# Optimization experiments

Hardware: AMD Instinct MI355X
Metric: run time of the kernel (lower is better)

## Reference

```python
import jax, jax.numpy as jnp
import numpy as np

COMMITMENT = 0.25  # beta


def setup_inputs() -> dict:
    key = jax.random.key(0)
    k1, k2 = jax.random.split(key)
    B, M, D, K = 16, 4096, 64, 1024
    z_e = jax.random.normal(k1, (B, M, D), dtype=jnp.float32)
    embed = jax.random.normal(k2, (K, D), dtype=jnp.float32)  # codebook C in R^{KxD}
    return {"z_e": z_e, "embed": embed}


def reference(z_e, embed):
    """Eval-mode VQ forward: nearest-code lookup + VQ loss + straight-through.

    z_e:   (B, M, D) encoder outputs
    embed: (K, D) codebook
    Returns (z_q_st, indices, vq_loss).
    """
    B, M, D = z_e.shape
    flat = z_e.reshape(-1, D)  # (N, D)
    dist = (
        jnp.sum(flat * flat, axis=1, keepdims=True)
        - 2.0 * (flat @ embed.T)
        + jnp.sum(embed * embed, axis=1)[None, :]
    )
    indices = jnp.argmin(dist, axis=1)  # (N,)
    z_q = embed[indices].reshape(B, M, D)  # gather

    sg = jax.lax.stop_gradient
    codebook_loss = jnp.mean((z_q - sg(z_e)) ** 2)
    commitment_loss = jnp.mean((z_e - sg(z_q)) ** 2)
    vq_loss = codebook_loss + COMMITMENT * commitment_loss

    z_q_st = z_e + sg(z_q - z_e)  # straight-through estimator
    return z_q_st, indices.reshape(B, M), vq_loss
```

## Files before the change

### kernel.cpp

```cpp
#include <hip/hip_runtime.h>
#include <hip/hip_bf16.h>
#include <stdint.h>

#define D_     64
#define K_     1024
#define N_     65536
#define TPB    64
#define RPB    16
#define NBLK   (N_ / RPB)
#define MARGIN 0.06f

typedef __bf16 bf16x8 __attribute__((ext_vector_type(8)));
typedef float  f32x4  __attribute__((ext_vector_type(4)));

__device__ __forceinline__ unsigned short bf16_rne(float f) {
    union { float f; uint32_t u; } v; v.f = f;
    const uint32_t u = v.u;
    return (unsigned short)((u + 0x7fffu + ((u >> 16) & 1u)) >> 16);
}
__device__ __forceinline__ float bf16_tof(unsigned short h) {
    union { uint32_t u; float f; } v; v.u = ((uint32_t)h) << 16;
    return v.f;
}

__global__ __launch_bounds__(64) void vq_prep(const float* __restrict__ embed,
                                              double* __restrict__ n64,
                                              float* __restrict__ n32,
                                              char* __restrict__ eb) {
    const int gid = blockIdx.x * 64 + threadIdx.x;
    const int k   = gid >> 2;
    const int q4  = gid & 3;
    const float4* e4 = (const float4*)(embed + (size_t)k * D_ + q4 * 16);
    double accA = 0.0, accB = 0.0;
    uint32_t hw[8], lw[8];
#pragma unroll
    for (int q = 0; q < 4; ++q) {
        const float4 e = e4[q];
        float c[4] = {e.x, e.y, e.z, e.w};
        unsigned short hb[4], lb[4];
#pragma unroll
        for (int j = 0; j < 4; ++j) {
            hb[j] = bf16_rne(c[j]);
            lb[j] = bf16_rne(c[j] - bf16_tof(hb[j]));
        }
        accA = fma((double)c[0], (double)c[0], accA);
        accB = fma((double)c[1], (double)c[1], accB);
        accA = fma((double)c[2], (double)c[2], accA);
        accB = fma((double)c[3], (double)c[3], accB);
        hw[q * 2]     = (uint32_t)hb[0] | ((uint32_t)hb[1] << 16);
        hw[q * 2 + 1] = (uint32_t)hb[2] | ((uint32_t)hb[3] << 16);
        lw[q * 2]     = (uint32_t)lb[0] | ((uint32_t)lb[1] << 16);
        lw[q * 2 + 1] = (uint32_t)lb[2] | ((uint32_t)lb[3] << 16);
    }
    double acc = accA + accB;
    acc += __shfl_xor(acc, 1);
    acc += __shfl_xor(acc, 2);
    if (q4 == 0) { n64[k] = acc; n32[k] = (float)acc; }
    const int ct = k >> 4, cl = k & 15;
    char* hp = eb + (size_t)ct * 4096        + (q4 * 16 + cl) * 32;
    char* lp = eb + (size_t)ct * 4096 + 2048 + (q4 * 16 + cl) * 32;
    int4 h0; h0.x = hw[0]; h0.y = hw[1]; h0.z = hw[2]; h0.w = hw[3];
    int4 h1; h1.x = hw[4]; h1.y = hw[5]; h1.z = hw[6]; h1.w = hw[7];
    int4 l0; l0.x = lw[0]; l0.y = lw[1]; l0.z = lw[2]; l0.w = lw[3];
    int4 l1; l1.x = lw[4]; l1.y = lw[5]; l1.z = lw[6]; l1.w = lw[7];
    *(int4*)hp = h0; *(int4*)(hp + 16) = h1;
    *(int4*)lp = l0; *(int4*)(lp + 16) = l1;
}

__global__ __launch_bounds__(TPB) void vq_main(const float* __restrict__ z_e,
                                               const float* __restrict__ embed,
                                               const char* __restrict__ eb,
                                               const float* __restrict__ n32g,
                                               const double* __restrict__ n64g,
                                               float* __restrict__ out,
                                               float* __restrict__ partials) {
    const int lane = threadIdx.x;
    const int lg   = lane >> 4;
    const int lc   = lane & 15;
    const int wrow0 = blockIdx.x * RPB;

    bf16x8 ah[2], al[2];
    {
        const float4* xg = (const float4*)(z_e + (size_t)(wrow0 + lc) * D_ + lg * 16);
        float xs[16];
#pragma unroll
        for (int q = 0; q < 4; ++q) {
            const float4 x = xg[q];
            xs[q * 4 + 0] = x.x; xs[q * 4 + 1] = x.y;
            xs[q * 4 + 2] = x.z; xs[q * 4 + 3] = x.w;
        }
#pragma unroll
        for (int s = 0; s < 2; ++s) {
#pragma unroll
            for (int i = 0; i < 8; ++i) {
                const float xf = xs[s * 8 + i];
                const unsigned short hb = bf16_rne(xf);
                const unsigned short lb = bf16_rne(xf - bf16_tof(hb));
                union { unsigned short u; __bf16 h; } uh, ul;
                uh.u = hb; ul.u = lb;
                ah[s][i] = uh.h;
                al[s][i] = ul.h;
            }
        }
    }

    float b1[4], b2[4];
    int   i1[4];
#pragma unroll
    for (int rg = 0; rg < 4; ++rg) { b1[rg] = 3.4e38f; b2[rg] = 3.4e38f; i1[rg] = 0; }

    const char* ebl = eb + lane * 32;

#define LOADPAIR(P, R) {                                                  \
        const char* p0_ = ebl + (size_t)(P) * 8192;                       \
        R##h00 = *(const int4*)(p0_);                                     \
        R##h01 = *(const int4*)(p0_ + 16);                                \
        R##l00 = *(const int4*)(p0_ + 2048);                              \
        R##l01 = *(const int4*)(p0_ + 2064);                              \
        R##h10 = *(const int4*)(p0_ + 4096);                              \
        R##h11 = *(const int4*)(p0_ + 4112);                              \
        R##l10 = *(const int4*)(p0_ + 6144);                              \
        R##l11 = *(const int4*)(p0_ + 6160);                              \
        R##nv0 = n32g[(P) * 32 + lc];                                     \
        R##nv1 = n32g[(P) * 32 + 16 + lc];                                \
    }
#define COMPGROUP(KI, H0, H1, L0, L1, NV) {                               \
        const bf16x8 bh0 = __builtin_bit_cast(bf16x8, H0);                \
        const bf16x8 bh1 = __builtin_bit_cast(bf16x8, H1);                \
        const bf16x8 bl0 = __builtin_bit_cast(bf16x8, L0);                \
        const bf16x8 bl1 = __builtin_bit_cast(bf16x8, L1);                \
        f32x4 acc0 = {0.f, 0.f, 0.f, 0.f};                                \
        f32x4 acc1 = {0.f, 0.f, 0.f, 0.f};                                \
        acc0 = __builtin_amdgcn_mfma_f32_16x16x32_bf16(ah[0], bh0, acc0, 0, 0, 0); \
        acc1 = __builtin_amdgcn_mfma_f32_16x16x32_bf16(ah[1], bh1, acc1, 0, 0, 0); \
        acc0 = __builtin_amdgcn_mfma_f32_16x16x32_bf16(al[0], bh0, acc0, 0, 0, 0); \
        acc1 = __builtin_amdgcn_mfma_f32_16x16x32_bf16(al[1], bh1, acc1, 0, 0, 0); \
        acc0 = __builtin_amdgcn_mfma_f32_16x16x32_bf16(ah[0], bl0, acc0, 0, 0, 0); \
        acc1 = __builtin_amdgcn_mfma_f32_16x16x32_bf16(ah[1], bl1, acc1, 0, 0, 0); \
        const int ki_ = (KI) + lc;                                        \
        _Pragma("unroll")                                                 \
        for (int rg = 0; rg < 4; ++rg) {                                  \
            const float s  = fmaf(-2.0f, acc0[rg] + acc1[rg], NV);        \
            const bool  lt = s < b1[rg];                                  \
            const float m2 = fminf(s, b2[rg]);                            \
            b2[rg] = lt ? b1[rg] : m2;                                    \
            b1[rg] = lt ? s      : b1[rg];                                \
            i1[rg] = lt ? ki_    : i1[rg];                                \
        }                                                                 \
    }
#define COMPPAIR(P, R) {                                                  \
        COMPGROUP((P) * 32,      R##h00, R##h01, R##l00, R##l01, R##nv0); \
        COMPGROUP((P) * 32 + 16, R##h10, R##h11, R##l10, R##l11, R##nv1); \
    }

    {
        int4 Ah00, Ah01, Al00, Al01, Ah10, Ah11, Al10, Al11; float Anv0, Anv1;
        int4 Bh00, Bh01, Bl00, Bl01, Bh10, Bh11, Bl10, Bl11; float Bnv0, Bnv1;
        LOADPAIR(0, A);
        for (int p = 0; p < 32; p += 2) {
            LOADPAIR(p + 1, B);
            COMPPAIR(p, A);
            const int np = (p + 2 < 32) ? (p + 2) : 0;
            LOADPAIR(np, A);
            COMPPAIR(p + 1, B);
        }
    }
#undef LOADPAIR
#undef COMPGROUP
#undef COMPPAIR

#pragma unroll
    for (int rg = 0; rg < 4; ++rg)
#pragma unroll
        for (int off = 1; off <= 8; off <<= 1) {
            const float ob1 = __shfl_xor(b1[rg], off);
            const float ob2 = __shfl_xor(b2[rg], off);
            const int   oi1 = __shfl_xor(i1[rg], off);
            if (ob1 < b1[rg] || (ob1 == b1[rg] && oi1 < i1[rg])) {
                b2[rg] = fminf(b1[rg], ob2); b1[rg] = ob1; i1[rg] = oi1;
            } else {
                b2[rg] = fminf(ob1, b2[rg]);
            }
        }

#pragma unroll
    for (int rg = 0; rg < 4; ++rg) {
        for (int g = 0; g < 4; ++g) {
            const float g1 = __shfl(b1[rg], g << 4);
            const float g2 = __shfl(b2[rg], g << 4);
            if (g2 - g1 < MARGIN) {
                const int grow = wrow0 + g * 4 + rg;
                const float* xp = z_e + (size_t)grow * D_;
                double bs = 1.0e300; int bi = 1 << 30;
                for (int c0 = 0; c0 < K_; c0 += 64) {
                    const int c = c0 + lane;
                    const float* ep = embed + (size_t)c * D_;
                    double dot = 0.0;
#pragma unroll
                    for (int j = 0; j < D_; ++j)
                        dot = fma((double)xp[j], (double)ep[j], dot);
                    const double sc = fma(-2.0, dot, n64g[c]);
                    if (sc < bs) { bs = sc; bi = c; }
                }
#pragma unroll
                for (int off = 32; off > 0; off >>= 1) {
                    const double so = __shfl_xor(bs, off);
                    const int    io = __shfl_xor(bi, off);
                    if (so < bs || (so == bs && io < bi)) { bs = so; bi = io; }
                }
                if (lg == g) i1[rg] = bi;
            }
        }
    }

    float sq = 0.f;
    {
        const int srcl = (lc >> 2) << 4;
        const int c0v = __shfl(i1[0], srcl);
        const int c1v = __shfl(i1[1], srcl);
        const int c2v = __shfl(i1[2], srcl);
        const int c3v = __shfl(i1[3], srcl);
        const int rsel = lc & 3;
        int bidx = (rsel == 0) ? c0v : (rsel == 1) ? c1v : (rsel == 2) ? c2v : c3v;
        bidx &= (K_ - 1);
        const int row = wrow0 + lc;
        const float4* eg = (const float4*)(embed + (size_t)bidx * D_ + lg * 16);
        const float4* xg = (const float4*)(z_e + (size_t)row * D_ + lg * 16);
        float4*       og = (float4*)(out + (size_t)row * D_ + lg * 16);
#pragma unroll
        for (int q = 0; q < 4; ++q) {
            const float4 e = eg[q];
            const float4 x = xg[q];
            const float d0 = e.x - x.x;
            const float d1 = e.y - x.y;
            const float d2 = e.z - x.z;
            const float d3 = e.w - x.w;
            sq = fmaf(d0, d0, sq); sq = fmaf(d1, d1, sq);
            sq = fmaf(d2, d2, sq); sq = fmaf(d3, d3, sq);
            float4 o;
            o.x = x.x + d0;
            o.y = x.y + d1;
            o.z = x.z + d2;
            o.w = x.w + d3;
            og[q] = o;
        }
        if (lg == 0) out[(size_t)N_ * D_ + row] = (float)bidx;
    }

#pragma unroll
    for (int off = 32; off > 0; off >>= 1) sq += __shfl_xor(sq, off);
    if (lane == 0) partials[blockIdx.x] = sq;
}

__global__ __launch_bounds__(256) void vq_loss_final(const float* __restrict__ partials,
                                                     float* __restrict__ out) {
    __shared__ float red[256];
    const int tid = threadIdx.x;
    float s = 0.f;
#pragma unroll
    for (int i = 0; i < NBLK / 256; ++i) s += partials[tid + i * 256];
    red[tid] = s;
    __syncthreads();
#pragma unroll
    for (int w = 128; w > 0; w >>= 1) {
        if (tid < w) red[tid] += red[tid + w];
        __syncthreads();
    }
    if (tid == 0)
        out[(size_t)N_ * D_ + N_] = 1.25f * red[0] / (float)((size_t)N_ * D_);
}

extern "C" void kernel_launch(void* const* d_in, const int* in_sizes, int n_in,
                              void* d_out, int out_size, void* d_ws, size_t ws_size,
                              hipStream_t stream) {
    const float* z_e;
    const float* embed;
    if (in_sizes[0] == N_ * D_) {
        z_e   = (const float*)d_in[0];
        embed = (const float*)d_in[1];
    } else {
        z_e   = (const float*)d_in[1];
        embed = (const float*)d_in[0];
    }
    float* out = (float*)d_out;

    double* n64      = (double*)d_ws;
    float*  n32      = (float*)(n64 + K_);
    float*  partials = n32 + K_;
    char*   eb       = (char*)(partials + NBLK);

    vq_prep<<<K_ / 16, 64, 0, stream>>>(embed, n64, n32, eb);
    vq_main<<<NBLK, TPB, 0, stream>>>(z_e, embed, eb, n32, n64, out, partials);
    vq_loss_final<<<1, 256, 0, stream>>>(partials, out);
}
```

Before: 193.5 us.

## Process two 16-row tiles per wave to reuse codebook fragments across rows

Each wave now handles 32 rows (two 16-row MFMA tiles) instead of 16, so every codebook fragment loaded from global memory feeds twice as many MFMAs. The packed codebook layout changes to 16-byte-per-lane chunks at 1 KB strides, and the loop walks 64 groups of 16 codes instead of 32 pairs. This halves the codebook traffic per row but doubles the accumulator and operand registers and halves the grid size, which may lower occupancy and parallelism.

```diff
diff --git a/kernel.cpp b/kernel.cpp
--- a/kernel.cpp
+++ b/kernel.cpp
@@ -6,7 +6,7 @@
 #define K_     1024
 #define N_     65536
 #define TPB    64
-#define RPB    16
+#define RPB    32
 #define NBLK   (N_ / RPB)
 #define MARGIN 0.06f
 
@@ -57,14 +57,15 @@
     acc += __shfl_xor(acc, 2);
     if (q4 == 0) { n64[k] = acc; n32[k] = (float)acc; }
     const int ct = k >> 4, cl = k & 15;
-    char* hp = eb + (size_t)ct * 4096        + (q4 * 16 + cl) * 32;
-    char* lp = eb + (size_t)ct * 4096 + 2048 + (q4 * 16 + cl) * 32;
+    char* base = eb + (size_t)ct * 4096 + (q4 * 16 + cl) * 16;
     int4 h0; h0.x = hw[0]; h0.y = hw[1]; h0.z = hw[2]; h0.w = hw[3];
     int4 h1; h1.x = hw[4]; h1.y = hw[5]; h1.z = hw[6]; h1.w = hw[7];
     int4 l0; l0.x = lw[0]; l0.y = lw[1]; l0.z = lw[2]; l0.w = lw[3];
     int4 l1; l1.x = lw[4]; l1.y = lw[5]; l1.z = lw[6]; l1.w = lw[7];
-    *(int4*)hp = h0; *(int4*)(hp + 16) = h1;
-    *(int4*)lp = l0; *(int4*)(lp + 16) = l1;
+    *(int4*)(base)        = h0;
+    *(int4*)(base + 1024) = h1;
+    *(int4*)(base + 2048) = l0;
+    *(int4*)(base + 3072) = l1;
 }
 
 __global__ __launch_bounds__(TPB) void vq_main(const float* __restrict__ z_e,
@@ -79,9 +80,10 @@
     const int lc   = lane & 15;
     const int wrow0 = blockIdx.x * RPB;
 
-    bf16x8 ah[2], al[2];
-    {
-        const float4* xg = (const float4*)(z_e + (size_t)(wrow0 + lc) * D_ + lg * 16);
+    bf16x8 ah[2][2], al[2][2];
+#pragma unroll
+    for (int t = 0; t < 2; ++t) {
+        const float4* xg = (const float4*)(z_e + (size_t)(wrow0 + t * 16 + lc) * D_ + lg * 16);
         float xs[16];
 #pragma unroll
         for (int q = 0; q < 4; ++q) {
@@ -98,132 +100,144 @@
                 const unsigned short lb = bf16_rne(xf - bf16_tof(hb));
                 union { unsigned short u; __bf16 h; } uh, ul;
                 uh.u = hb; ul.u = lb;
-                ah[s][i] = uh.h;
-                al[s][i] = ul.h;
+                ah[t][s][i] = uh.h;
+                al[t][s][i] = ul.h;
             }
         }
     }
 
-    float b1[4], b2[4];
-    int   i1[4];
-#pragma unroll
-    for (int rg = 0; rg < 4; ++rg) { b1[rg] = 3.4e38f; b2[rg] = 3.4e38f; i1[rg] = 0; }
-
-    const char* ebl = eb + lane * 32;
-
-#define LOADPAIR(P, R) {                                                  \
-        const char* p0_ = ebl + (size_t)(P) * 8192;                       \
-        R##h00 = *(const int4*)(p0_);                                     \
-        R##h01 = *(const int4*)(p0_ + 16);                                \
-        R##l00 = *(const int4*)(p0_ + 2048);                              \
-        R##l01 = *(const int4*)(p0_ + 2064);                              \
-        R##h10 = *(const int4*)(p0_ + 4096);                              \
-        R##h11 = *(const int4*)(p0_ + 4112);                              \
-        R##l10 = *(const int4*)(p0_ + 6144);                              \
-        R##l11 = *(const int4*)(p0_ + 6160);                              \
-        R##nv0 = n32g[(P) * 32 + lc];                                     \
-        R##nv1 = n32g[(P) * 32 + 16 + lc];                                \
-    }
-#define COMPGROUP(KI, H0, H1, L0, L1, NV) {                               \
-        const bf16x8 bh0 = __builtin_bit_cast(bf16x8, H0);                \
-        const bf16x8 bh1 = __builtin_bit_cast(bf16x8, H1);                \
-        const bf16x8 bl0 = __builtin_bit_cast(bf16x8, L0);                \
-        const bf16x8 bl1 = __builtin_bit_cast(bf16x8, L1);                \
-        f32x4 acc0 = {0.f, 0.f, 0.f, 0.f};                                \
-        f32x4 acc1 = {0.f, 0.f, 0.f, 0.f};                                \
-        acc0 = __builtin_amdgcn_mfma_f32_16x16x32_bf16(ah[0], bh0, acc0, 0, 0, 0); \
-        acc1 = __builtin_amdgcn_mfma_f32_16x16x32_bf16(ah[1], bh1, acc1, 0, 0, 0); \
-        acc0 = __builtin_amdgcn_mfma_f32_16x16x32_bf16(al[0], bh0, acc0, 0, 0, 0); \
-        acc1 = __builtin_amdgcn_mfma_f32_16x16x32_bf16(al[1], bh1, acc1, 0, 0, 0); \
-        acc0 = __builtin_amdgcn_mfma_f32_16x16x32_bf16(ah[0], bl0, acc0, 0, 0, 0); \
-        acc1 = __builtin_amdgcn_mfma_f32_16x16x32_bf16(ah[1], bl1, acc1, 0, 0, 0); \
+    float b1[2][4], b2[2][4];
+    int   i1[2][4];
+#pragma unroll
+    for (int t = 0; t < 2; ++t)
+#pragma unroll
+        for (int rg = 0; rg < 4; ++rg) { b1[t][rg] = 3.4e38f; b2[t][rg] = 3.4e38f; i1[t][rg] = 0; }
+
+    const char* ebl = eb + lane * 16;
+
+#define LOADG(G, R) {                                                     \
+        const char* p_ = ebl + (size_t)(G) * 4096;                        \
+        R##h0 = *(const int4*)(p_);                                       \
+        R##h1 = *(const int4*)(p_ + 1024);                                \
+        R##l0 = *(const int4*)(p_ + 2048);                                \
+        R##l1 = *(const int4*)(p_ + 3072);                                \
+        R##nv = n32g[(G) * 16 + lc];                                      \
+    }
+#define COMPG(KI, R) {                                                    \
+        const bf16x8 bh0 = __builtin_bit_cast(bf16x8, R##h0);             \
+        const bf16x8 bh1 = __builtin_bit_cast(bf16x8, R##h1);             \
+        const bf16x8 bl0 = __builtin_bit_cast(bf16x8, R##l0);             \
+        const bf16x8 bl1 = __builtin_bit_cast(bf16x8, R##l1);             \
+        f32x4 a00 = {0.f, 0.f, 0.f, 0.f};                                 \
+        f32x4 a01 = {0.f, 0.f, 0.f, 0.f};                                 \
+        f32x4 a10 = {0.f, 0.f, 0.f, 0.f};                                 \
+        f32x4 a11 = {0.f, 0.f, 0.f, 0.f};                                 \
+        a00 = __builtin_amdgcn_mfma_f32_16x16x32_bf16(ah[0][0], bh0, a00, 0, 0, 0); \
+        a01 = __builtin_amdgcn_mfma_f32_16x16x32_bf16(ah[0][1], bh1, a01, 0, 0, 0); \
+        a10 = __builtin_amdgcn_mfma_f32_16x16x32_bf16(ah[1][0], bh0, a10, 0, 0, 0); \
+        a11 = __builtin_amdgcn_mfma_f32_16x16x32_bf16(ah[1][1], bh1, a11, 0, 0, 0); \
+        a00 = __builtin_amdgcn_mfma_f32_16x16x32_bf16(al[0][0], bh0, a00, 0, 0, 0); \
+        a01 = __builtin_amdgcn_mfma_f32_16x16x32_bf16(al[0][1], bh1, a01, 0, 0, 0); \
+        a10 = __builtin_amdgcn_mfma_f32_16x16x32_bf16(al[1][0], bh0, a10, 0, 0, 0); \
+        a11 = __builtin_amdgcn_mfma_f32_16x16x32_bf16(al[1][1], bh1, a11, 0, 0, 0); \
+        a00 = __builtin_amdgcn_mfma_f32_16x16x32_bf16(ah[0][0], bl0, a00, 0, 0, 0); \
+        a01 = __builtin_amdgcn_mfma_f32_16x16x32_bf16(ah[0][1], bl1, a01, 0, 0, 0); \
+        a10 = __builtin_amdgcn_mfma_f32_16x16x32_bf16(ah[1][0], bl0, a10, 0, 0, 0); \
+        a11 = __builtin_amdgcn_mfma_f32_16x16x32_bf16(ah[1][1], bl1, a11, 0, 0, 0); \
         const int ki_ = (KI) + lc;                                        \
         _Pragma("unroll")                                                 \
         for (int rg = 0; rg < 4; ++rg) {                                  \
-            const float s  = fmaf(-2.0f, acc0[rg] + acc1[rg], NV);        \
-            const bool  lt = s < b1[rg];                                  \
-            const float m2 = fminf(s, b2[rg]);                            \
-            b2[rg] = lt ? b1[rg] : m2;                                    \
-            b1[rg] = lt ? s      : b1[rg];                                \
-            i1[rg] = lt ? ki_    : i1[rg];                                \
+            const float s0 = fmaf(-2.0f, a00[rg] + a01[rg], R##nv);       \
+            const float s1 = fmaf(-2.0f, a10[rg] + a11[rg], R##nv);       \
+            const bool  lt0 = s0 < b1[0][rg];                             \
+            const float m20 = fminf(s0, b2[0][rg]);                       \
+            b2[0][rg] = lt0 ? b1[0][rg] : m20;                            \
+            b1[0][rg] = lt0 ? s0        : b1[0][rg];                      \
+            i1[0][rg] = lt0 ? ki_       : i1[0][rg];                      \
+            const bool  lt1 = s1 < b1[1][rg];                             \
+            const float m21 = fminf(s1, b2[1][rg]);                       \
+            b2[1][rg] = lt1 ? b1[1][rg] : m21;                            \
+            b1[1][rg] = lt1 ? s1        : b1[1][rg];                      \
+            i1[1][rg] = lt1 ? ki_       : i1[1][rg];                      \
         }                                                                 \
     }
-#define COMPPAIR(P, R) {                                                  \
-        COMPGROUP((P) * 32,      R##h00, R##h01, R##l00, R##l01, R##nv0); \
-        COMPGROUP((P) * 32 + 16, R##h10, R##h11, R##l10, R##l11, R##nv1); \
-    }
 
     {
-        int4 Ah00, Ah01, Al00, Al01, Ah10, Ah11, Al10, Al11; float Anv0, Anv1;
-        int4 Bh00, Bh01, Bl00, Bl01, Bh10, Bh11, Bl10, Bl11; float Bnv0, Bnv1;
-        LOADPAIR(0, A);
-        for (int p = 0; p < 32; p += 2) {
-            LOADPAIR(p + 1, B);
-            COMPPAIR(p, A);
-            const int np = (p + 2 < 32) ? (p + 2) : 0;
-            LOADPAIR(np, A);
-            COMPPAIR(p + 1, B);
-        }
-    }
-#undef LOADPAIR
-#undef COMPGROUP
-#undef COMPPAIR
-
-#pragma unroll
-    for (int rg = 0; rg < 4; ++rg)
-#pragma unroll
-        for (int off = 1; off <= 8; off <<= 1) {
-            const float ob1 = __shfl_xor(b1[rg], off);
-            const float ob2 = __shfl_xor(b2[rg], off);
-            const int   oi1 = __shfl_xor(i1[rg], off);
-            if (ob1 < b1[rg] || (ob1 == b1[rg] && oi1 < i1[rg])) {
-                b2[rg] = fminf(b1[rg], ob2); b1[rg] = ob1; i1[rg] = oi1;
-            } else {
-                b2[rg] = fminf(ob1, b2[rg]);
+        int4 Ah0, Ah1, Al0, Al1; float Anv;
+        int4 Bh0, Bh1, Bl0, Bl1; float Bnv;
+        LOADG(0, A);
+        for (int g = 0; g < 64; g += 2) {
+            LOADG(g + 1, B);
+            COMPG(g * 16, A);
+            const int ng = (g + 2 < 64) ? (g + 2) : 0;
+            LOADG(ng, A);
+            COMPG((g + 1) * 16, B);
+        }
+    }
+#undef LOADG
+#undef COMPG
+
+#pragma unroll
+    for (int t = 0; t < 2; ++t)
+#pragma unroll
+        for (int rg = 0; rg < 4; ++rg)
+#pragma unroll
+            for (int off = 1; off <= 8; off <<= 1) {
+                const float ob1 = __shfl_xor(b1[t][rg], off);
+                const float ob2 = __shfl_xor(b2[t][rg], off);
+                const int   oi1 = __shfl_xor(i1[t][rg], off);
+                if (ob1 < b1[t][rg] || (ob1 == b1[t][rg] && oi1 < i1[t][rg])) {
+                    b2[t][rg] = fminf(b1[t][rg], ob2); b1[t][rg] = ob1; i1[t][rg] = oi1;
+                } else {
+                    b2[t][rg] = fminf(ob1, b2[t][rg]);
+                }
             }
-        }
-
-#pragma unroll
-    for (int rg = 0; rg < 4; ++rg) {
-        for (int g = 0; g < 4; ++g) {
-            const float g1 = __shfl(b1[rg], g << 4);
-            const float g2 = __shfl(b2[rg], g << 4);
-            if (g2 - g1 < MARGIN) {
-                const int grow = wrow0 + g * 4 + rg;
-                const float* xp = z_e + (size_t)grow * D_;
-                double bs = 1.0e300; int bi = 1 << 30;
-                for (int c0 = 0; c0 < K_; c0 += 64) {
-                    const int c = c0 + lane;
-                    const float* ep = embed + (size_t)c * D_;
-                    double dot = 0.0;
-#pragma unroll
-                    for (int j = 0; j < D_; ++j)
-                        dot = fma((double)xp[j], (double)ep[j], dot);
-                    const double sc = fma(-2.0, dot, n64g[c]);
-                    if (sc < bs) { bs = sc; bi = c; }
+
+#pragma unroll
+    for (int t = 0; t < 2; ++t) {
+#pragma unroll
+        for (int rg = 0; rg < 4; ++rg) {
+            for (int g = 0; g < 4; ++g) {
+                const float g1 = __shfl(b1[t][rg], g << 4);
+                const float g2 = __shfl(b2[t][rg], g << 4);
+                if (g2 - g1 < MARGIN) {
+                    const int grow = wrow0 + t * 16 + g * 4 + rg;
+                    const float* xp = z_e + (size_t)grow * D_;
+                    double bs = 1.0e300; int bi = 1 << 30;
+                    for (int c0 = 0; c0 < K_; c0 += 64) {
+                        const int c = c0 + lane;
+                        const float* ep = embed + (size_t)c * D_;
+                        double dot = 0.0;
+#pragma unroll
+                        for (int j = 0; j < D_; ++j)
+                            dot = fma((double)xp[j], (double)ep[j], dot);
+                        const double sc = fma(-2.0, dot, n64g[c]);
+                        if (sc < bs) { bs = sc; bi = c; }
+                    }
+#pragma unroll
+                    for (int off = 32; off > 0; off >>= 1) {
+                        const double so = __shfl_xor(bs, off);
+                        const int    io = __shfl_xor(bi, off);
+                        if (so < bs || (so == bs && io < bi)) { bs = so; bi = io; }
+                    }
+                    if (lg == g) i1[t][rg] = bi;
                 }
-#pragma unroll
-                for (int off = 32; off > 0; off >>= 1) {
-                    const double so = __shfl_xor(bs, off);
-                    const int    io = __shfl_xor(bi, off);
-                    if (so < bs || (so == bs && io < bi)) { bs = so; bi = io; }
-                }
-                if (lg == g) i1[rg] = bi;
             }
         }
     }
 
     float sq = 0.f;
-    {
+#pragma unroll
+    for (int t = 0; t < 2; ++t) {
         const int srcl = (lc >> 2) << 4;
-        const int c0v = __shfl(i1[0], srcl);
-        const int c1v = __shfl(i1[1], srcl);
-        const int c2v = __shfl(i1[2], srcl);
-        const int c3v = __shfl(i1[3], srcl);
+        const int c0v = __shfl(i1[t][0], srcl);
+        const int c1v = __shfl(i1[t][1], srcl);
+        const int c2v = __shfl(i1[t][2], srcl);
+        const int c3v = __shfl(i1[t][3], srcl);
         const int rsel = lc & 3;
         int bidx = (rsel == 0) ? c0v : (rsel == 1) ? c1v : (rsel == 2) ? c2v : c3v;
         bidx &= (K_ - 1);
-        const int row = wrow0 + lc;
+        const int row = wrow0 + t * 16 + lc;
         const float4* eg = (const float4*)(embed + (size_t)bidx * D_ + lg * 16);
         const float4* xg = (const float4*)(z_e + (size_t)row * D_ + lg * 16);
         float4*       og = (float4*)(out + (size_t)row * D_ + lg * 16);
```

Result: no change. 196.0 us (+1.3%).

## Repack codebook layout for coalesced loads and break MFMA accumulator chains

Applied to the files above, without the earlier changes.

The codebook prep kernel now stores each 16-code tile as four contiguous 1 KB planes (hi/lo × two K-halves), so each lane loads 16 bytes at stride 16 and every load instruction is fully coalesced. The main loop double-buffers one 16-code group at a time instead of pairs of groups, which lowers register pressure. The six MFMAs per group now write independent accumulators and are summed afterwards, removing the dependent accumulate chain so the MFMAs can issue back to back. The cost is a few extra adds per row group and a different rounding order in the dot-product sum.

```diff
diff --git a/kernel.cpp b/kernel.cpp
--- a/kernel.cpp
+++ b/kernel.cpp
@@ -57,14 +57,15 @@
     acc += __shfl_xor(acc, 2);
     if (q4 == 0) { n64[k] = acc; n32[k] = (float)acc; }
     const int ct = k >> 4, cl = k & 15;
-    char* hp = eb + (size_t)ct * 4096        + (q4 * 16 + cl) * 32;
-    char* lp = eb + (size_t)ct * 4096 + 2048 + (q4 * 16 + cl) * 32;
+    char* base = eb + (size_t)ct * 4096 + (q4 * 16 + cl) * 16;
     int4 h0; h0.x = hw[0]; h0.y = hw[1]; h0.z = hw[2]; h0.w = hw[3];
     int4 h1; h1.x = hw[4]; h1.y = hw[5]; h1.z = hw[6]; h1.w = hw[7];
     int4 l0; l0.x = lw[0]; l0.y = lw[1]; l0.z = lw[2]; l0.w = lw[3];
     int4 l1; l1.x = lw[4]; l1.y = lw[5]; l1.z = lw[6]; l1.w = lw[7];
-    *(int4*)hp = h0; *(int4*)(hp + 16) = h1;
-    *(int4*)lp = l0; *(int4*)(lp + 16) = l1;
+    *(int4*)(base)        = h0;
+    *(int4*)(base + 1024) = h1;
+    *(int4*)(base + 2048) = l0;
+    *(int4*)(base + 3072) = l1;
 }
 
 __global__ __launch_bounds__(TPB) void vq_main(const float* __restrict__ z_e,
@@ -109,38 +110,39 @@
 #pragma unroll
     for (int rg = 0; rg < 4; ++rg) { b1[rg] = 3.4e38f; b2[rg] = 3.4e38f; i1[rg] = 0; }
 
-    const char* ebl = eb + lane * 32;
-
-#define LOADPAIR(P, R) {                                                  \
-        const char* p0_ = ebl + (size_t)(P) * 8192;                       \
-        R##h00 = *(const int4*)(p0_);                                     \
-        R##h01 = *(const int4*)(p0_ + 16);                                \
-        R##l00 = *(const int4*)(p0_ + 2048);                              \
-        R##l01 = *(const int4*)(p0_ + 2064);                              \
-        R##h10 = *(const int4*)(p0_ + 4096);                              \
-        R##h11 = *(const int4*)(p0_ + 4112);                              \
-        R##l10 = *(const int4*)(p0_ + 6144);                              \
-        R##l11 = *(const int4*)(p0_ + 6160);                              \
-        R##nv0 = n32g[(P) * 32 + lc];                                     \
-        R##nv1 = n32g[(P) * 32 + 16 + lc];                                \
-    }
-#define COMPGROUP(KI, H0, H1, L0, L1, NV) {                               \
-        const bf16x8 bh0 = __builtin_bit_cast(bf16x8, H0);                \
-        const bf16x8 bh1 = __builtin_bit_cast(bf16x8, H1);                \
-        const bf16x8 bl0 = __builtin_bit_cast(bf16x8, L0);                \
-        const bf16x8 bl1 = __builtin_bit_cast(bf16x8, L1);                \
-        f32x4 acc0 = {0.f, 0.f, 0.f, 0.f};                                \
-        f32x4 acc1 = {0.f, 0.f, 0.f, 0.f};                                \
-        acc0 = __builtin_amdgcn_mfma_f32_16x16x32_bf16(ah[0], bh0, acc0, 0, 0, 0); \
-        acc1 = __builtin_amdgcn_mfma_f32_16x16x32_bf16(ah[1], bh1, acc1, 0, 0, 0); \
-        acc0 = __builtin_amdgcn_mfma_f32_16x16x32_bf16(al[0], bh0, acc0, 0, 0, 0); \
-        acc1 = __builtin_amdgcn_mfma_f32_16x16x32_bf16(al[1], bh1, acc1, 0, 0, 0); \
-        acc0 = __builtin_amdgcn_mfma_f32_16x16x32_bf16(ah[0], bl0, acc0, 0, 0, 0); \
-        acc1 = __builtin_amdgcn_mfma_f32_16x16x32_bf16(ah[1], bl1, acc1, 0, 0, 0); \
+    const char* ebl = eb + lane * 16;
+
+#define LOADG(G, R) {                                                     \
+        const char* p_ = ebl + (size_t)(G) * 4096;                        \
+        R##h0 = *(const int4*)(p_);                                       \
+        R##h1 = *(const int4*)(p_ + 1024);                                \
+        R##l0 = *(const int4*)(p_ + 2048);                                \
+        R##l1 = *(const int4*)(p_ + 3072);                                \
+        R##nv = n32g[(G) * 16 + lc];                                      \
+    }
+#define COMPG(KI, R) {                                                    \
+        const bf16x8 bh0 = __builtin_bit_cast(bf16x8, R##h0);             \
+        const bf16x8 bh1 = __builtin_bit_cast(bf16x8, R##h1);             \
+        const bf16x8 bl0 = __builtin_bit_cast(bf16x8, R##l0);             \
+        const bf16x8 bl1 = __builtin_bit_cast(bf16x8, R##l1);             \
+        f32x4 c0 = {0.f, 0.f, 0.f, 0.f};                                  \
+        f32x4 c1 = {0.f, 0.f, 0.f, 0.f};                                  \
+        f32x4 c2 = {0.f, 0.f, 0.f, 0.f};                                  \
+        f32x4 c3 = {0.f, 0.f, 0.f, 0.f};                                  \
+        f32x4 c4 = {0.f, 0.f, 0.f, 0.f};                                  \
+        f32x4 c5 = {0.f, 0.f, 0.f, 0.f};                                  \
+        c0 = __builtin_amdgcn_mfma_f32_16x16x32_bf16(ah[0], bh0, c0, 0, 0, 0); \
+        c1 = __builtin_amdgcn_mfma_f32_16x16x32_bf16(ah[1], bh1, c1, 0, 0, 0); \
+        c2 = __builtin_amdgcn_mfma_f32_16x16x32_bf16(al[0], bh0, c2, 0, 0, 0); \
+        c3 = __builtin_amdgcn_mfma_f32_16x16x32_bf16(al[1], bh1, c3, 0, 0, 0); \
+        c4 = __builtin_amdgcn_mfma_f32_16x16x32_bf16(ah[0], bl0, c4, 0, 0, 0); \
+        c5 = __builtin_amdgcn_mfma_f32_16x16x32_bf16(ah[1], bl1, c5, 0, 0, 0); \
         const int ki_ = (KI) + lc;                                        \
         _Pragma("unroll")                                                 \
         for (int rg = 0; rg < 4; ++rg) {                                  \
-            const float s  = fmaf(-2.0f, acc0[rg] + acc1[rg], NV);        \
+            const float sum = ((c0[rg] + c1[rg]) + (c2[rg] + c3[rg]))     \
+                              + (c4[rg] + c5[rg]);                        \
+            const float s  = fmaf(-2.0f, sum, R##nv);                     \
             const bool  lt = s < b1[rg];                                  \
             const float m2 = fminf(s, b2[rg]);                            \
             b2[rg] = lt ? b1[rg] : m2;                                    \
@@ -148,26 +150,21 @@
             i1[rg] = lt ? ki_    : i1[rg];                                \
         }                                                                 \
     }
-#define COMPPAIR(P, R) {                                                  \
-        COMPGROUP((P) * 32,      R##h00, R##h01, R##l00, R##l01, R##nv0); \
-        COMPGROUP((P) * 32 + 16, R##h10, R##h11, R##l10, R##l11, R##nv1); \
-    }
 
     {
-        int4 Ah00, Ah01, Al00, Al01, Ah10, Ah11, Al10, Al11; float Anv0, Anv1;
-        int4 Bh00, Bh01, Bl00, Bl01, Bh10, Bh11, Bl10, Bl11; float Bnv0, Bnv1;
-        LOADPAIR(0, A);
-        for (int p = 0; p < 32; p += 2) {
-            LOADPAIR(p + 1, B);
-            COMPPAIR(p, A);
-            const int np = (p + 2 < 32) ? (p + 2) : 0;
-            LOADPAIR(np, A);
-            COMPPAIR(p + 1, B);
-        }
-    }
-#undef LOADPAIR
-#undef COMPGROUP
-#undef COMPPAIR
+        int4 Ah0, Ah1, Al0, Al1; float Anv;
+        int4 Bh0, Bh1, Bl0, Bl1; float Bnv;
+        LOADG(0, A);
+        for (int g = 0; g < 64; g += 2) {
+            LOADG(g + 1, B);
+            COMPG(g * 16, A);
+            const int ng = (g + 2 < 64) ? (g + 2) : 0;
+            LOADG(ng, A);
+            COMPG((g + 1) * 16, B);
+        }
+    }
+#undef LOADG
+#undef COMPG
 
 #pragma unroll
     for (int rg = 0; rg < 4; ++rg)
```

New measurement: 200.7 us. 3.7% more time.
